# Kernel tuning notes

Measured on AMD Instinct MI355X. Metric: run time of the kernel, lower is better.

## Reference

```python
import jax, jax.numpy as jnp
import numpy as np

B, N_PER_G, DEG = 128, 1024, 8
N = B * N_PER_G
E = N * DEG
IN_DIM, HID, OUT_DIM = 128, 64, 10
EPS = 1e-5


def _gcn(x, src, dst, ew, W, b, n_nodes):
    # GCNConv with add_self_loops=True, symmetric normalization, edge weights ew in {0,1}
    xw = x @ W                                                 # [N, HID]
    deg = jax.ops.segment_sum(ew, dst, num_segments=n_nodes) + 1.0  # +1 self loop
    dinv = jax.lax.rsqrt(deg)
    norm = dinv[src] * dinv[dst] * ew                          # [E]
    agg = jax.ops.segment_sum(xw[src] * norm[:, None], dst, num_segments=n_nodes)
    return agg + xw * (dinv * dinv)[:, None] + b               # self-loop term + bias


def _bn_relu(x, g, beta):
    # BatchNorm1d training-mode stats over node dim (biased var), then ReLU
    mu = x.mean(0)
    var = ((x - mu) ** 2).mean(0)
    return jax.nn.relu((x - mu) * jax.lax.rsqrt(var + EPS) * g + beta)


def _topk_pool(x, src, dst, ew, p, n_per_g):
    # PyG TopKPooling: score = x.p/||p||, keep top ceil(0.8*n) per graph, x *= tanh(score)
    k = (4 * n_per_g + 4) // 5  # ceil(0.8 * n), static
    score = (x @ p) / jnp.linalg.norm(p)                       # [B*n]
    _, idx = jax.lax.top_k(score.reshape(B, n_per_g), k)       # [B, k] local indices
    perm = (idx + (jnp.arange(B) * n_per_g)[:, None]).reshape(-1)  # [B*k] global
    xs = x[perm] * jnp.tanh(score[perm])[:, None]
    # re-index edges; edges touching dropped nodes get weight 0 (mask, fixed E)
    mapping = jnp.full((B * n_per_g,), -1, jnp.int32).at[perm].set(
        jnp.arange(B * k, dtype=jnp.int32))
    ns, nd = mapping[src], mapping[dst]
    valid = (ns >= 0) & (nd >= 0) & (ew > 0)
    return xs, jnp.where(valid, ns, 0), jnp.where(valid, nd, 0), valid.astype(x.dtype), k


def _readout(x, k):
    xg = x.reshape(B, k, HID)
    return jnp.concatenate([xg.mean(1), xg.max(1)], axis=1)    # [B, 2*HID]


def _forward(x, edge_index, W1, b1, gamma1, beta1, p1, W2, b2, gamma2, beta2, p2,
             W3, b3, gamma3, beta3, p3, Wm, bm):
    src, dst = edge_index[0], edge_index[1]
    ew = jnp.ones((E,), x.dtype)
    n = N_PER_G
    blocks = [(W1, b1, gamma1, beta1, p1),
              (W2, b2, gamma2, beta2, p2),
              (W3, b3, gamma3, beta3, p3)]
    readout = jnp.zeros((B, 2 * HID), x.dtype)
    for W, b, g, bt, p in blocks:
        h = _gcn(x, src, dst, ew, W, b, B * n)
        h = _bn_relu(h, g, bt)
        x, src, dst, ew, n = _topk_pool(h, src, dst, ew, p, n)
        readout = readout + _readout(x, n)
    return readout @ Wm + bm                                   # [B, OUT_DIM]


def setup_inputs():
    key = jax.random.key(0)
    ks = jax.random.split(key, 20)
    x = jax.random.normal(ks[0], (N, IN_DIM), jnp.float32)
    src_l = jax.random.randint(ks[1], (E,), 0, N_PER_G)
    dst_l = jax.random.randint(ks[2], (E,), 0, N_PER_G)
    off = jnp.repeat(jnp.arange(B, dtype=jnp.int32) * N_PER_G, N_PER_G * DEG)
    edge_index = jnp.stack([src_l.astype(jnp.int32) + off,
                            dst_l.astype(jnp.int32) + off])   # [2, E] intra-graph
    d = {"x": x, "edge_index": edge_index}
    dims = [(IN_DIM, HID), (HID, HID), (HID, HID)]
    for i, (di, do) in enumerate(dims, 1):
        d[f"W{i}"] = jax.random.normal(ks[3 * i], (di, do), jnp.float32) / np.sqrt(di)
        d[f"b{i}"] = jnp.zeros((do,), jnp.float32)
        d[f"gamma{i}"] = jnp.ones((do,), jnp.float32)
        d[f"beta{i}"] = jnp.zeros((do,), jnp.float32)
        d[f"p{i}"] = jax.random.normal(ks[3 * i + 1], (do,), jnp.float32)
    d["Wm"] = jax.random.normal(ks[15], (2 * HID, OUT_DIM), jnp.float32) / np.sqrt(2 * HID)
    d["bm"] = jnp.zeros((OUT_DIM,), jnp.float32)
    return d


def reference(x, edge_index, W1, b1, gamma1, beta1, p1, W2, b2, gamma2, beta2, p2,
              W3, b3, gamma3, beta3, p3, Wm, bm):
    return _forward(x, edge_index, W1, b1, gamma1, beta1, p1,
                    W2, b2, gamma2, beta2, p2, W3, b3, gamma3, beta3, p3, Wm, bm)
```

## Files before the change

kernel.cpp:

```cpp
#include <hip/hip_runtime.h>
#include <cmath>
#include <cstdint>
#include <cstddef>

#define HID 64
#define NGR 128
#define NTOT 131072
#define EDGES 1048576
#define EPG 8192

__global__ __launch_bounds__(256) void pack_init(
    const int* __restrict__ ei, uint32_t* __restrict__ packed,
    uint16_t* __restrict__ csr_g, uint32_t* __restrict__ rs_g,
    float* __restrict__ dinv_g, float* __restrict__ sums3,
    float* __restrict__ readout) {
  __shared__ int hist[1024];
  __shared__ int part[256];
  __shared__ int cursor[1024];
  int b = blockIdx.x, t = threadIdx.x;
  for (int i = t; i < 1024; i += 256) hist[i] = 0;
  __syncthreads();
  int ebase = b * EPG, nbase = b << 10;
  for (int e = t; e < EPG; e += 256) {
    uint32_t s = (uint32_t)(ei[ebase + e] - nbase);
    uint32_t d = (uint32_t)(ei[EDGES + ebase + e] - nbase);
    packed[ebase + e] = s | (d << 10);
    atomicAdd(&hist[(int)d], 1);
  }
  __syncthreads();
  int h0 = hist[t * 4], h1 = hist[t * 4 + 1], h2 = hist[t * 4 + 2], h3 = hist[t * 4 + 3];
  int tot = h0 + h1 + h2 + h3;
  part[t] = tot;
  __syncthreads();
  for (int off = 1; off < 256; off <<= 1) {
    int v = (t >= off) ? part[t - off] : 0;
    __syncthreads();
    part[t] += v;
    __syncthreads();
  }
  int excl = part[t] - tot;
  int r0 = excl, r1 = r0 + h0, r2 = r1 + h1, r3 = r2 + h2;
  cursor[t * 4 + 0] = r0; cursor[t * 4 + 1] = r1;
  cursor[t * 4 + 2] = r2; cursor[t * 4 + 3] = r3;
  uint32_t* rg = rs_g + b * 1025;
  rg[t * 4 + 0] = r0; rg[t * 4 + 1] = r1; rg[t * 4 + 2] = r2; rg[t * 4 + 3] = r3;
  if (t == 255) rg[1024] = EPG;
  for (int i = t; i < 1024; i += 256)
    dinv_g[(b << 10) + i] = rsqrtf((float)hist[i] + 1.0f);
  __syncthreads();
  for (int e = t; e < EPG; e += 256) {
    uint32_t pk = packed[ebase + e];
    int d = (pk >> 10) & 1023;
    int idx = atomicAdd(&cursor[d], 1);
    csr_g[ebase + idx] = (uint16_t)(pk & 1023);
  }
  if (b < 3 && t < 128) sums3[b * 128 + t] = 0.0f;
  if (t < 128) readout[b * 128 + t] = 0.0f;
}

template<int DIN, bool TIN>
__global__ __launch_bounds__(256) void gemm_xw(
    const float* __restrict__ X, const float* __restrict__ W,
    float* __restrict__ XWT, int n_nodes) {
  __shared__ float sW[32 * HID];
  __shared__ float sX[32 * 132];
  const int t = threadIdx.x;
  const int cq = t & 15, ng = t >> 4;
  const int c4 = cq * 4;
  const int node0 = blockIdx.x * 128;
  const size_t Nn = (size_t)n_nodes;
  float acc[8][4];
#pragma unroll
  for (int n = 0; n < 8; n++) { acc[n][0]=0.f; acc[n][1]=0.f; acc[n][2]=0.f; acc[n][3]=0.f; }

  for (int k0 = 0; k0 < DIN; k0 += 32) {
    ((float4*)sW)[t * 2 + 0] = ((const float4*)(W + (size_t)k0 * HID))[t * 2 + 0];
    ((float4*)sW)[t * 2 + 1] = ((const float4*)(W + (size_t)k0 * HID))[t * 2 + 1];
    if (TIN) {
#pragma unroll
      for (int it = 0; it < 4; it++) {
        int slot = t + it * 256;
        int row = slot >> 5, col4 = (slot & 31) * 4;
        *(float4*)(sX + row * 132 + col4) =
            *(const float4*)(X + (size_t)(k0 + row) * Nn + node0 + col4);
      }
    } else {
      int i4 = (t & 7) * 4;
      int nl = t >> 3;
#pragma unroll
      for (int rep = 0; rep < 4; rep++) {
        int nn = nl + rep * 32;
        float4 v = *(const float4*)(X + (size_t)(node0 + nn) * DIN + k0 + i4);
        sX[(i4 + 0) * 132 + nn] = v.x;
        sX[(i4 + 1) * 132 + nn] = v.y;
        sX[(i4 + 2) * 132 + nn] = v.z;
        sX[(i4 + 3) * 132 + nn] = v.w;
      }
    }
    __syncthreads();
#pragma unroll 4
    for (int i = 0; i < 32; i++) {
      float4 w = *(const float4*)(sW + i * HID + c4);
      const float* xr = sX + i * 132 + ng * 8;
      float4 xa = *(const float4*)xr;
      float4 xb = *(const float4*)(xr + 4);
      float xn[8] = {xa.x, xa.y, xa.z, xa.w, xb.x, xb.y, xb.z, xb.w};
#pragma unroll
      for (int n = 0; n < 8; n++) {
        acc[n][0] = fmaf(xn[n], w.x, acc[n][0]);
        acc[n][1] = fmaf(xn[n], w.y, acc[n][1]);
        acc[n][2] = fmaf(xn[n], w.z, acc[n][2]);
        acc[n][3] = fmaf(xn[n], w.w, acc[n][3]);
      }
    }
    __syncthreads();
  }
#pragma unroll
  for (int cc = 0; cc < 4; cc++) {
    int row = c4 + cc;
    float* o = XWT + (size_t)row * Nn + node0 + ng * 8;
    *(float4*)(o + 0) = make_float4(acc[0][cc], acc[1][cc], acc[2][cc], acc[3][cc]);
    *(float4*)(o + 4) = make_float4(acc[4][cc], acc[5][cc], acc[6][cc], acc[7][cc]);
  }
}

__global__ __launch_bounds__(1024, 8) void edge_agg(
    const uint16_t* __restrict__ csr_g, const uint32_t* __restrict__ rs_g,
    const float* __restrict__ dinv_g, const float* __restrict__ xwT,
    const float* __restrict__ bias, float* __restrict__ hT,
    float* __restrict__ sums) {
  __shared__ float xws[8 * 1028];
  __shared__ float dv[1024];
  __shared__ uint32_t rs[1025];
  __shared__ uint16_t csr_s[8192];
  __shared__ float sredS[16][8], sredQ[16][8];
  const int g = blockIdx.x & 127;
  const int q = blockIdx.x >> 7;
  const int c0 = q * 8;
  const int t = threadIdx.x;
  const int gbase = g << 10;

  dv[t] = dinv_g[gbase + t];
  if (t < 1024) rs[t] = rs_g[g * 1025 + t];
  if (t == 0) rs[1024] = EPG;
  ((uint4*)csr_s)[t] = ((const uint4*)(csr_g + (size_t)g * EPG))[t];
  for (int slot = t; slot < 2048; slot += 1024) {
    int c = slot >> 8, pos4 = (slot & 255) * 4;
    float4 v = *(const float4*)(xwT + (size_t)(c0 + c) * NTOT + gbase + pos4);
    float4 dd = *(const float4*)(dinv_g + gbase + pos4);
    v.x *= dd.x; v.y *= dd.y; v.z *= dd.z; v.w *= dd.w;
    *(float4*)(xws + c * 1028 + pos4) = v;
  }
  __syncthreads();

  const int c = t & 7, j = t >> 3;
  const float* xc = xws + c * 1028;
  const float bv = bias[c0 + c];
  float* hrow = hT + (size_t)(c0 + c) * NTOT + gbase;
  float S = 0.0f, Q = 0.0f;
  for (int d = j; d < 1024; d += 128) {
    float dvd = dv[d];
    if (dvd == 0.0f) continue;
    int e = rs[d], e1 = rs[d + 1];
    float a0 = 0.0f, a1 = 0.0f;
    for (; e + 2 <= e1; e += 2) {
      int s0 = csr_s[e], s1 = csr_s[e + 1];
      a0 += xc[s0];
      a1 += xc[s1];
    }
    if (e < e1) a0 += xc[csr_s[e]];
    float hv = (a0 + a1 + xc[d]) * dvd + bv;
    hrow[d] = hv;
    S += hv; Q += hv * hv;
  }
#pragma unroll
  for (int m = 8; m < 64; m <<= 1) { S += __shfl_xor(S, m); Q += __shfl_xor(Q, m); }
  {
    int lane = t & 63, w = t >> 6;
    if (lane < 8) { sredS[w][lane] = S; sredQ[w][lane] = Q; }
  }
  __syncthreads();
  if (t < 8) {
    float a = 0.0f;
    for (int w2 = 0; w2 < 16; w2++) a += sredS[w2][t];
    atomicAdd(&sums[c0 + t], a);
  } else if (t < 16) {
    int cc = t - 8;
    float a = 0.0f;
    for (int w2 = 0; w2 < 16; w2++) a += sredQ[w2][cc];
    atomicAdd(&sums[64 + cc + c0], a);
  }
}

__global__ __launch_bounds__(256) void score_kernel(
    const float* __restrict__ hT, const float* __restrict__ sums,
    const float* __restrict__ gamma, const float* __restrict__ beta,
    const float* __restrict__ p, const float* __restrict__ dinv_g,
    float* __restrict__ score, float* __restrict__ stanh_g, float inv_n) {
  __shared__ float ssc[64], ssh[64], sp[64];
  __shared__ float sipn;
  int b = blockIdx.x >> 2, seg = (blockIdx.x & 3) << 8;
  int t = threadIdx.x;
  int node = (b << 10) + seg + t;
  if (t < 64) {
    float mu = sums[t] * inv_n;
    float var = fmaxf(sums[64 + t] * inv_n - mu * mu, 0.0f);
    float sc = rsqrtf(var + 1e-5f) * gamma[t];
    ssc[t] = sc; ssh[t] = beta[t] - mu * sc;
    sp[t] = p[t];
  }
  __syncthreads();
  if (t == 0) {
    float s = 0.0f;
    for (int i = 0; i < 64; i++) s += sp[i] * sp[i];
    sipn = rsqrtf(s);
  }
  __syncthreads();
  const float* hp = hT + node;
  float s0 = 0.0f;
#pragma unroll 16
  for (int c = 0; c < 64; c++) {
    float y = fmaxf(fmaf(hp[(size_t)c * NTOT], ssc[c], ssh[c]), 0.0f);
    s0 = fmaf(y, sp[c], s0);
  }
  float v0 = s0 * sipn;
  score[node] = (dinv_g[node] > 0.0f) ? v0 : -INFINITY;
  stanh_g[node] = tanhf(v0);
}

__global__ __launch_bounds__(1024) void topk_kernel(
    const float* __restrict__ score, int* __restrict__ snext_g, int k) {
  __shared__ float __align__(16) ssc2[4 * 260];
  int b = blockIdx.x >> 2, p = blockIdx.x & 3;
  int t = threadIdx.x;
  int gbase = b << 10;
  float sv = score[gbase + t];
  ssc2[(t >> 8) * 260 + (t & 255)] = sv;
  __syncthreads();
  int il = t >> 2, jq = t & 3;
  int gi = p * 256 + il;
  float my = ssc2[(gi >> 8) * 260 + (gi & 255)];
  const float4* base = (const float4*)(ssc2 + jq * 260);
  int jbase = jq * 256;
  int r = 0;
#pragma unroll 8
  for (int m = 0; m < 64; m++) {
    float4 v = base[m];
    int j0 = jbase + m * 4;
    r += (v.x > my) || (v.x == my && (j0 + 0) < gi);
    r += (v.y > my) || (v.y == my && (j0 + 1) < gi);
    r += (v.z > my) || (v.z == my && (j0 + 2) < gi);
    r += (v.w > my) || (v.w == my && (j0 + 3) < gi);
  }
  r += __shfl_xor(r, 1);
  r += __shfl_xor(r, 2);
  if (jq == 0) snext_g[gbase + gi] = (r < k) ? 1 : 0;
}

__global__ __launch_bounds__(256) void pool_kernel(
    const float* __restrict__ hT, const float* __restrict__ sums,
    const float* __restrict__ gamma, const float* __restrict__ beta,
    const float* __restrict__ stanh_g, const int* __restrict__ snext_g,
    const uint16_t* __restrict__ csr_g, const uint32_t* __restrict__ rs_g,
    float* __restrict__ xT_out, float* __restrict__ dinv_g,
    float* __restrict__ readout, int k, float inv_n, int hasNext) {
  __shared__ float ssc[64], ssh[64];
  __shared__ float sth[1024];
  __shared__ int skn[1024];
  __shared__ float redS[4][8], redM[4][8];
  int g = blockIdx.x & 127, q = blockIdx.x >> 7;
  int t = threadIdx.x;
  int gbase = g << 10;
  if (t < 64) {
    float mu = sums[t] * inv_n;
    float var = fmaxf(sums[64 + t] * inv_n - mu * mu, 0.0f);
    float sc = rsqrtf(var + 1e-5f) * gamma[t];
    ssc[t] = sc; ssh[t] = beta[t] - mu * sc;
  }
  for (int i = t; i < 1024; i += 256) {
    sth[i] = stanh_g[gbase + i];
    skn[i] = snext_g[gbase + i];
  }
  __syncthreads();
  int lane = t & 63, w = t >> 6;
#pragma unroll
  for (int i = 0; i < 8; i++) {
    int c = q * 8 + i;
    const float* hrow = hT + (size_t)c * NTOT + gbase;
    float* xrow = xT_out ? (xT_out + (size_t)c * NTOT + gbase) : nullptr;
    float scc = ssc[c], shh = ssh[c];
    float S = 0.0f, M = -INFINITY;
    for (int nd = t; nd < 1024; nd += 256) {
      bool kn = skn[nd] != 0;
      float y = fmaxf(fmaf(hrow[nd], scc, shh), 0.0f) * sth[nd];
      y = kn ? y : 0.0f;
      if (xrow) xrow[nd] = y;
      S += y;
      if (kn) M = fmaxf(M, y);
    }
#pragma unroll
    for (int m = 1; m < 64; m <<= 1) {
      S += __shfl_xor(S, m);
      M = fmaxf(M, __shfl_xor(M, m));
    }
    if (lane == 0) { redS[w][i] = S; redM[w][i] = M; }
  }
  if (hasNext && t < 128) {
    int d = q * 128 + t;
    if (skn[d]) {
      uint32_t e0 = rs_g[g * 1025 + d], e1 = rs_g[g * 1025 + d + 1];
      const uint16_t* row = csr_g + (size_t)g * EPG;
      int cnt = 0;
      for (uint32_t e = e0; e < e1; e++) cnt += skn[row[e]];
      dinv_g[gbase + d] = rsqrtf((float)cnt + 1.0f);
    } else {
      dinv_g[gbase + d] = 0.0f;
    }
  }
  __syncthreads();
  if (t < 8) {
    float S = redS[0][t] + redS[1][t] + redS[2][t] + redS[3][t];
    readout[g * 128 + q * 8 + t] += S / (float)k;
  } else if (t < 16) {
    int i = t - 8;
    float M = fmaxf(fmaxf(redM[0][i], redM[1][i]), fmaxf(redM[2][i], redM[3][i]));
    readout[g * 128 + 64 + q * 8 + i] += M;
  }
}

__global__ __launch_bounds__(256) void final_linear(
    const float* __restrict__ readout, const float* __restrict__ Wm,
    const float* __restrict__ bm, float* __restrict__ out) {
  int idx = blockIdx.x * 256 + threadIdx.x;
  if (idx >= NGR * 10) return;
  int b = idx / 10, o = idx - b * 10;
  float acc = bm[o];
  const float* r = readout + (size_t)b * 128;
  for (int c = 0; c < 128; c++) acc = fmaf(r[c], Wm[c * 10 + o], acc);
  out[idx] = acc;
}

extern "C" void kernel_launch(void* const* d_in, const int* in_sizes, int n_in,
                              void* d_out, int out_size, void* d_ws, size_t ws_size,
                              hipStream_t stream) {
  (void)in_sizes; (void)n_in; (void)out_size; (void)ws_size;
  const float* x  = (const float*)d_in[0];
  const int*   ei = (const int*)d_in[1];
  const float* Wk[3]  = {(const float*)d_in[2],  (const float*)d_in[7],  (const float*)d_in[12]};
  const float* bk[3]  = {(const float*)d_in[3],  (const float*)d_in[8],  (const float*)d_in[13]};
  const float* gk[3]  = {(const float*)d_in[4],  (const float*)d_in[9],  (const float*)d_in[14]};
  const float* btk[3] = {(const float*)d_in[5],  (const float*)d_in[10], (const float*)d_in[15]};
  const float* pk[3]  = {(const float*)d_in[6],  (const float*)d_in[11], (const float*)d_in[16]};
  const float* Wm = (const float*)d_in[17];
  const float* bm = (const float*)d_in[18];
  float* out = (float*)d_out;

  float* ws = (float*)d_ws;
  size_t off = 0;
  auto alloc = [&](size_t nfl) {
    float* ptr = ws + off;
    off += (nfl + 63) & ~(size_t)63;
    return ptr;
  };
  float* bufXW = alloc((size_t)NTOT * 64);
  float* bufH  = alloc((size_t)NTOT * 64);
  float* bufX  = alloc((size_t)NTOT * 64);
  float* dinv_g = alloc(NTOT);
  float* score  = alloc(NTOT);
  float* stanh_g = alloc(NTOT);
  int*   snext_g = (int*)alloc(NTOT);
  uint32_t* packed = (uint32_t*)alloc(EDGES);
  uint16_t* csr    = (uint16_t*)alloc(EDGES / 2);
  uint32_t* rs     = (uint32_t*)alloc(NGR * 1025);
  float* sums3 = alloc(3 * 128);
  float* readout = alloc(NGR * 2 * HID);

  pack_init<<<NGR, 256, 0, stream>>>(ei, packed, csr, rs, dinv_g, sums3, readout);

  const int   kk[3] = {820, 656, 525};
  const float invn[3] = {1.0f / (float)NTOT, 1.0f / (float)(NGR * 820),
                         1.0f / (float)(NGR * 656)};

  for (int L = 0; L < 3; L++) {
    float* sums = sums3 + L * 128;
    if (L == 0)
      gemm_xw<128, false><<<NTOT / 128, 256, 0, stream>>>(x, Wk[0], bufXW, NTOT);
    else
      gemm_xw<64, true><<<NTOT / 128, 256, 0, stream>>>(bufX, Wk[L], bufXW, NTOT);
    edge_agg<<<8 * NGR, 1024, 0, stream>>>(csr, rs, dinv_g, bufXW, bk[L], bufH, sums);
    score_kernel<<<4 * NGR, 256, 0, stream>>>(bufH, sums, gk[L], btk[L], pk[L],
                                              dinv_g, score, stanh_g, invn[L]);
    topk_kernel<<<4 * NGR, 1024, 0, stream>>>(score, snext_g, kk[L]);
    pool_kernel<<<8 * NGR, 256, 0, stream>>>(bufH, sums, gk[L], btk[L],
                                             stanh_g, snext_g, csr, rs,
                                             (L < 2) ? bufX : nullptr, dinv_g,
                                             readout, kk[L], invn[L],
                                             (L < 2) ? 1 : 0);
  }
  final_linear<<<5, 256, 0, stream>>>(readout, Wm, bm, out);
}
```

Measured before the change: 486.4 us.

## Pad CSR rows to even length and enlarge GEMM register tile

Each destination's CSR row is padded to an even length with a sentinel index that points at a zeroed slot in shared memory. This lets edge_agg read two 16-bit source indices per 32-bit load with no scalar tail. Separately, the XW GEMM tile grows to 256 nodes by 64 columns per block, with each thread holding an 8x8 accumulator, to raise arithmetic per shared-memory load. The costs are more shared memory and registers (fewer blocks per CU), padding in the CSR, and a sentinel entry that the pool kernel must treat as not kept.

Result: faster. 472.4 us (-2.9%).

```diff
diff --git a/kernel.cpp b/kernel.cpp
--- a/kernel.cpp
+++ b/kernel.cpp
@@ -8,6 +8,8 @@
 #define NTOT 131072
 #define EDGES 1048576
 #define EPG 8192
+#define CPAD 9216
+#define SENT 1024
 
 __global__ __launch_bounds__(256) void pack_init(
     const int* __restrict__ ei, uint32_t* __restrict__ packed,
@@ -29,7 +31,8 @@
   }
   __syncthreads();
   int h0 = hist[t * 4], h1 = hist[t * 4 + 1], h2 = hist[t * 4 + 2], h3 = hist[t * 4 + 3];
-  int tot = h0 + h1 + h2 + h3;
+  int p0 = h0 + (h0 & 1), p1 = h1 + (h1 & 1), p2 = h2 + (h2 & 1), p3 = h3 + (h3 & 1);
+  int tot = p0 + p1 + p2 + p3;
   part[t] = tot;
   __syncthreads();
   for (int off = 1; off < 256; off <<= 1) {
@@ -39,86 +42,89 @@
     __syncthreads();
   }
   int excl = part[t] - tot;
-  int r0 = excl, r1 = r0 + h0, r2 = r1 + h1, r3 = r2 + h2;
+  int r0 = excl, r1 = r0 + p0, r2 = r1 + p1, r3 = r2 + p2;
   cursor[t * 4 + 0] = r0; cursor[t * 4 + 1] = r1;
   cursor[t * 4 + 2] = r2; cursor[t * 4 + 3] = r3;
   uint32_t* rg = rs_g + b * 1025;
   rg[t * 4 + 0] = r0; rg[t * 4 + 1] = r1; rg[t * 4 + 2] = r2; rg[t * 4 + 3] = r3;
-  if (t == 255) rg[1024] = EPG;
+  if (t == 255) rg[1024] = part[255];
   for (int i = t; i < 1024; i += 256)
     dinv_g[(b << 10) + i] = rsqrtf((float)hist[i] + 1.0f);
   __syncthreads();
+  uint16_t* cg = csr_g + (size_t)b * CPAD;
   for (int e = t; e < EPG; e += 256) {
     uint32_t pk = packed[ebase + e];
     int d = (pk >> 10) & 1023;
     int idx = atomicAdd(&cursor[d], 1);
-    csr_g[ebase + idx] = (uint16_t)(pk & 1023);
-  }
+    cg[idx] = (uint16_t)(pk & 1023);
+  }
+  __syncthreads();
+  for (int d = t; d < 1024; d += 256)
+    if (hist[d] & 1) cg[cursor[d]] = (uint16_t)SENT;
   if (b < 3 && t < 128) sums3[b * 128 + t] = 0.0f;
   if (t < 128) readout[b * 128 + t] = 0.0f;
 }
 
 template<int DIN, bool TIN>
-__global__ __launch_bounds__(256) void gemm_xw(
+__global__ __launch_bounds__(256, 2) void gemm_xw(
     const float* __restrict__ X, const float* __restrict__ W,
     float* __restrict__ XWT, int n_nodes) {
-  __shared__ float sW[32 * HID];
-  __shared__ float sX[32 * 132];
+  __shared__ float sW[32 * 64];
+  __shared__ float sX[32 * 260];
   const int t = threadIdx.x;
-  const int cq = t & 15, ng = t >> 4;
-  const int c4 = cq * 4;
-  const int node0 = blockIdx.x * 128;
+  const int c8 = (t & 7) * 8;
+  const int n8 = (t >> 3) * 8;
+  const int node0 = blockIdx.x * 256;
   const size_t Nn = (size_t)n_nodes;
-  float acc[8][4];
-#pragma unroll
-  for (int n = 0; n < 8; n++) { acc[n][0]=0.f; acc[n][1]=0.f; acc[n][2]=0.f; acc[n][3]=0.f; }
+  float acc[8][8];
+#pragma unroll
+  for (int n = 0; n < 8; n++)
+#pragma unroll
+    for (int c = 0; c < 8; c++) acc[n][c] = 0.0f;
 
   for (int k0 = 0; k0 < DIN; k0 += 32) {
-    ((float4*)sW)[t * 2 + 0] = ((const float4*)(W + (size_t)k0 * HID))[t * 2 + 0];
-    ((float4*)sW)[t * 2 + 1] = ((const float4*)(W + (size_t)k0 * HID))[t * 2 + 1];
+    ((float4*)sW)[t]       = ((const float4*)(W + (size_t)k0 * HID))[t];
+    ((float4*)sW)[t + 256] = ((const float4*)(W + (size_t)k0 * HID))[t + 256];
     if (TIN) {
 #pragma unroll
-      for (int it = 0; it < 4; it++) {
+      for (int it = 0; it < 8; it++) {
         int slot = t + it * 256;
-        int row = slot >> 5, col4 = (slot & 31) * 4;
-        *(float4*)(sX + row * 132 + col4) =
+        int row = slot >> 6, col4 = (slot & 63) * 4;
+        *(float4*)(sX + row * 260 + col4) =
             *(const float4*)(X + (size_t)(k0 + row) * Nn + node0 + col4);
       }
     } else {
-      int i4 = (t & 7) * 4;
-      int nl = t >> 3;
-#pragma unroll
-      for (int rep = 0; rep < 4; rep++) {
-        int nn = nl + rep * 32;
-        float4 v = *(const float4*)(X + (size_t)(node0 + nn) * DIN + k0 + i4);
-        sX[(i4 + 0) * 132 + nn] = v.x;
-        sX[(i4 + 1) * 132 + nn] = v.y;
-        sX[(i4 + 2) * 132 + nn] = v.z;
-        sX[(i4 + 3) * 132 + nn] = v.w;
+      int i4 = (t & 7) * 4, nn = t >> 3;
+#pragma unroll
+      for (int rep = 0; rep < 8; rep++) {
+        int node = nn + rep * 32;
+        float4 v = *(const float4*)(X + (size_t)(node0 + node) * DIN + k0 + i4);
+        sX[(i4 + 0) * 260 + node] = v.x;
+        sX[(i4 + 1) * 260 + node] = v.y;
+        sX[(i4 + 2) * 260 + node] = v.z;
+        sX[(i4 + 3) * 260 + node] = v.w;
       }
     }
     __syncthreads();
 #pragma unroll 4
     for (int i = 0; i < 32; i++) {
-      float4 w = *(const float4*)(sW + i * HID + c4);
-      const float* xr = sX + i * 132 + ng * 8;
-      float4 xa = *(const float4*)xr;
-      float4 xb = *(const float4*)(xr + 4);
-      float xn[8] = {xa.x, xa.y, xa.z, xa.w, xb.x, xb.y, xb.z, xb.w};
-#pragma unroll
-      for (int n = 0; n < 8; n++) {
-        acc[n][0] = fmaf(xn[n], w.x, acc[n][0]);
-        acc[n][1] = fmaf(xn[n], w.y, acc[n][1]);
-        acc[n][2] = fmaf(xn[n], w.z, acc[n][2]);
-        acc[n][3] = fmaf(xn[n], w.w, acc[n][3]);
-      }
+      float4 w0 = *(const float4*)(sW + i * 64 + c8);
+      float4 w1 = *(const float4*)(sW + i * 64 + c8 + 4);
+      float4 x0 = *(const float4*)(sX + i * 260 + n8);
+      float4 x1 = *(const float4*)(sX + i * 260 + n8 + 4);
+      float xn[8] = {x0.x, x0.y, x0.z, x0.w, x1.x, x1.y, x1.z, x1.w};
+      float wn[8] = {w0.x, w0.y, w0.z, w0.w, w1.x, w1.y, w1.z, w1.w};
+#pragma unroll
+      for (int n = 0; n < 8; n++)
+#pragma unroll
+        for (int c = 0; c < 8; c++)
+          acc[n][c] = fmaf(xn[n], wn[c], acc[n][c]);
     }
     __syncthreads();
   }
 #pragma unroll
-  for (int cc = 0; cc < 4; cc++) {
-    int row = c4 + cc;
-    float* o = XWT + (size_t)row * Nn + node0 + ng * 8;
+  for (int cc = 0; cc < 8; cc++) {
+    float* o = XWT + (size_t)(c8 + cc) * Nn + node0 + n8;
     *(float4*)(o + 0) = make_float4(acc[0][cc], acc[1][cc], acc[2][cc], acc[3][cc]);
     *(float4*)(o + 4) = make_float4(acc[4][cc], acc[5][cc], acc[6][cc], acc[7][cc]);
   }
@@ -132,7 +138,7 @@
   __shared__ float xws[8 * 1028];
   __shared__ float dv[1024];
   __shared__ uint32_t rs[1025];
-  __shared__ uint16_t csr_s[8192];
+  __shared__ uint32_t csr_s[CPAD / 2];
   __shared__ float sredS[16][8], sredQ[16][8];
   const int g = blockIdx.x & 127;
   const int q = blockIdx.x >> 7;
@@ -141,9 +147,13 @@
   const int gbase = g << 10;
 
   dv[t] = dinv_g[gbase + t];
-  if (t < 1024) rs[t] = rs_g[g * 1025 + t];
-  if (t == 0) rs[1024] = EPG;
-  ((uint4*)csr_s)[t] = ((const uint4*)(csr_g + (size_t)g * EPG))[t];
+  rs[t] = rs_g[g * 1025 + t];
+  if (t == 0) rs[1024] = rs_g[g * 1025 + 1024];
+  {
+    const uint4* src4 = (const uint4*)(csr_g + (size_t)g * CPAD);
+    ((uint4*)csr_s)[t] = src4[t];
+    if (t < CPAD / 8 - 1024) ((uint4*)csr_s)[1024 + t] = src4[1024 + t];
+  }
   for (int slot = t; slot < 2048; slot += 1024) {
     int c = slot >> 8, pos4 = (slot & 255) * 4;
     float4 v = *(const float4*)(xwT + (size_t)(c0 + c) * NTOT + gbase + pos4);
@@ -151,6 +161,7 @@
     v.x *= dd.x; v.y *= dd.y; v.z *= dd.z; v.w *= dd.w;
     *(float4*)(xws + c * 1028 + pos4) = v;
   }
+  if (t < 32) xws[(t >> 2) * 1028 + 1024 + (t & 3)] = 0.0f;
   __syncthreads();
 
   const int c = t & 7, j = t >> 3;
@@ -161,14 +172,14 @@
   for (int d = j; d < 1024; d += 128) {
     float dvd = dv[d];
     if (dvd == 0.0f) continue;
-    int e = rs[d], e1 = rs[d + 1];
+    int e  = rs[d] >> 1;
+    int e1 = rs[d + 1] >> 1;
     float a0 = 0.0f, a1 = 0.0f;
-    for (; e + 2 <= e1; e += 2) {
-      int s0 = csr_s[e], s1 = csr_s[e + 1];
-      a0 += xc[s0];
-      a1 += xc[s1];
-    }
-    if (e < e1) a0 += xc[csr_s[e]];
+    for (; e < e1; e++) {
+      uint32_t pk = csr_s[e];
+      a0 += xc[pk & 0xFFFFu];
+      a1 += xc[pk >> 16];
+    }
     float hv = (a0 + a1 + xc[d]) * dvd + bv;
     hrow[d] = hv;
     S += hv; Q += hv * hv;
@@ -266,7 +277,7 @@
     float* __restrict__ readout, int k, float inv_n, int hasNext) {
   __shared__ float ssc[64], ssh[64];
   __shared__ float sth[1024];
-  __shared__ int skn[1024];
+  __shared__ int skn[1025];
   __shared__ float redS[4][8], redM[4][8];
   int g = blockIdx.x & 127, q = blockIdx.x >> 7;
   int t = threadIdx.x;
@@ -281,6 +292,7 @@
     sth[i] = stanh_g[gbase + i];
     skn[i] = snext_g[gbase + i];
   }
+  if (t == 0) skn[1024] = 0;
   __syncthreads();
   int lane = t & 63, w = t >> 6;
 #pragma unroll
@@ -309,7 +321,7 @@
     int d = q * 128 + t;
     if (skn[d]) {
       uint32_t e0 = rs_g[g * 1025 + d], e1 = rs_g[g * 1025 + d + 1];
-      const uint16_t* row = csr_g + (size_t)g * EPG;
+      const uint16_t* row = csr_g + (size_t)g * CPAD;
       int cnt = 0;
       for (uint32_t e = e0; e < e1; e++) cnt += skn[row[e]];
       dinv_g[gbase + d] = rsqrtf((float)cnt + 1.0f);
@@ -370,7 +382,7 @@
   float* stanh_g = alloc(NTOT);
   int*   snext_g = (int*)alloc(NTOT);
   uint32_t* packed = (uint32_t*)alloc(EDGES);
-  uint16_t* csr    = (uint16_t*)alloc(EDGES / 2);
+  uint16_t* csr    = (uint16_t*)alloc((size_t)NGR * CPAD / 2);
   uint32_t* rs     = (uint32_t*)alloc(NGR * 1025);
   float* sums3 = alloc(3 * 128);
   float* readout = alloc(NGR * 2 * HID);
@@ -384,9 +396,9 @@
   for (int L = 0; L < 3; L++) {
     float* sums = sums3 + L * 128;
     if (L == 0)
-      gemm_xw<128, false><<<NTOT / 128, 256, 0, stream>>>(x, Wk[0], bufXW, NTOT);
+      gemm_xw<128, false><<<NTOT / 256, 256, 0, stream>>>(x, Wk[0], bufXW, NTOT);
     else
-      gemm_xw<64, true><<<NTOT / 128, 256, 0, stream>>>(bufX, Wk[L], bufXW, NTOT);
+      gemm_xw<64, true><<<NTOT / 256, 256, 0, stream>>>(bufX, Wk[L], bufXW, NTOT);
     edge_agg<<<8 * NGR, 1024, 0, stream>>>(csr, rs, dinv_g, bufXW, bk[L], bufH, sums);
     score_kernel<<<4 * NGR, 256, 0, stream>>>(bufH, sums, gk[L], btk[L], pk[L],
                                               dinv_g, score, stanh_g, invn[L]);
```
